# Performance work log

Measured on AMD Instinct MI355X. Metric: run time of the kernel, lower is better.

Reference implementation:

```python
import jax, jax.numpy as jnp
import numpy as np

B, T, D, H, L, S = 128, 100, 256, 512, 40000, 10  # batch, steps, input_size, hidden_size, loc_count, num_slots


def setup_inputs() -> dict:
    key = jax.random.key(0)
    ks = jax.random.split(key, 24)
    stdv = 1.0 / np.sqrt(H)
    u = lambda k, shape: jax.random.uniform(k, shape, jnp.float32, -stdv, stdv)
    inp = {
        "batch_l": jax.random.randint(ks[0], (B, T), 0, L),
        "t_ld": jax.random.uniform(ks[1], (B, T), jnp.float32),
        "t_hd": jax.random.uniform(ks[2], (B, T), jnp.float32),
        "t_l": jax.random.randint(ks[3], (B, T), 0, S),
        "t_h": jax.random.randint(ks[4], (B, T), 0, S),
        "d_ld": jax.random.uniform(ks[5], (B, T), jnp.float32),
        "d_hd": jax.random.uniform(ks[6], (B, T), jnp.float32),
        "d_l": jax.random.randint(ks[7], (B, T), 0, S),
        "d_h": jax.random.randint(ks[8], (B, T), 0, S),
        # learned parameters
        "embed_l": jax.random.normal(ks[9], (L, D), jnp.float32) * 0.02,
        "embed_s": jax.random.normal(ks[10], (S, D), jnp.float32) * 0.02,
        "embed_q": jax.random.normal(ks[11], (S, D), jnp.float32) * 0.02,
        "w_ih": u(ks[12], (4 * H, D)),
        "w_hh": u(ks[13], (4 * H, H)),
        "w_s": u(ks[14], (3 * H, D)),
        "w_q": u(ks[15], (3 * H, D)),
        "b_ih": u(ks[16], (4 * H,)),
        "b_hh": u(ks[17], (4 * H,)),
        "w_out": u(ks[18], (L, H)),
        "b_out": u(ks[19], (L,)),
    }
    return inp


def reference(batch_l, t_ld, t_hd, t_l, t_h, d_ld, d_hd, d_l, d_h,
              embed_l, embed_s, embed_q, w_ih, w_hh, w_s, w_q,
              b_ih, b_hh, w_out, b_out):
    # embedding lookups + slot interpolation: lower_embed*hd + higher_embed*ld
    xl = embed_l[batch_l]                                           # (B,T,D)
    xs = embed_s[d_l] * d_hd[..., None] + embed_s[d_h] * d_ld[..., None]
    xq = embed_q[t_l] * t_hd[..., None] + embed_q[t_h] * t_ld[..., None]

    def step(hc, x):
        h, c = hc
        xl_t, xs_t, xq_t = x                                        # each (B,D)
        gates = xl_t @ w_ih.T + h @ w_hh.T + b_ih + b_hh            # (B,4H)
        i, f, g, o = jnp.split(gates, 4, axis=1)
        sq = xs_t @ w_s.T + xq_t @ w_q.T                            # (B,3H), order (i,f,o)
        si, sf, so = jnp.split(sq, 3, axis=1)
        i = jax.nn.sigmoid(i + si)
        f = jax.nn.sigmoid(f + sf)
        o = jax.nn.sigmoid(o + so)
        g = jnp.tanh(g)
        c2 = f * c + i * g
        h2 = o * jnp.tanh(g)  # faithful to source: tanh(cell_gate), not tanh(next_cell)
        return (h2, c2), None

    h0 = jnp.zeros((B, H), xl.dtype)
    (hT, cT), _ = jax.lax.scan(
        step, (h0, h0),
        (xl.transpose(1, 0, 2), xs.transpose(1, 0, 2), xq.transpose(1, 0, 2)))
    # classifier on last hidden state
    return hT @ w_out.T + b_out                                     # (B,L)
```

## Files before the change

### kernel.cpp

```cpp
#include <hip/hip_runtime.h>

#define B_ 128
#define T_ 100
#define D_ 256
#define H_ 512
#define L_ 40000
#define S_ 10

__device__ __forceinline__ float sigm_(float x){ return 1.f/(1.f + __expf(-x)); }
__device__ __forceinline__ float tanh_(float x){ return 1.f - 2.f/(__expf(2.f*x) + 1.f); }

typedef __attribute__((ext_vector_type(8))) short bf16x8;
typedef __attribute__((ext_vector_type(4))) float f32x4;

__device__ __forceinline__ unsigned short bfhi_(float x){
  unsigned u = __float_as_uint(x);
  return (unsigned short)((u + 0x7FFFu + ((u >> 16) & 1u)) >> 16);
}
__device__ __forceinline__ float bf2f_(unsigned short h){
  return __uint_as_float(((unsigned)h) << 16);
}
__device__ __forceinline__ float decp_(unsigned u){
  return bf2f_((unsigned short)(u & 0xFFFFu)) + bf2f_((unsigned short)(u >> 16));
}

__global__ void k_init(unsigned long long* __restrict__ h_enc, unsigned* __restrict__ flags,
                       const float* __restrict__ embed_s, const float* __restrict__ embed_q,
                       const float* __restrict__ w_s, const float* __restrict__ w_q,
                       float* __restrict__ es_proj, float* __restrict__ eq_proj){
  int bid = blockIdx.x, tid = threadIdx.x;
  if (bid < 256){ h_enc[bid*256 + tid] = 0ull; return; }
  if (bid == 256){ if (tid < 256) flags[tid] = 0u; return; }
  int b2 = bid - 257;
  int table = b2/20, rem = b2%20, s = rem/2, half = rem%2;
  int jo = half*256 + tid;
  const float* emb = (table ? embed_q : embed_s) + s*D_;
  const float* w   = (table ? w_q : w_s) + (size_t)(2*H_ + jo)*D_;
  float acc = 0.f;
  #pragma unroll 4
  for (int k=0;k<D_;++k) acc = fmaf(emb[k], w[k], acc);
  (table ? eq_proj : es_proj)[s*H_ + jo] = acc;
}

__global__ __launch_bounds__(256) void k_conv_w(
  const float* __restrict__ w_ih,
  unsigned short* __restrict__ Whi, unsigned short* __restrict__ Wlo)
{
  int g = blockIdx.x*256 + threadIdx.x;
  size_t row = (size_t)(g >> 6), k4 = (size_t)(g & 63)*4;
  const float* src = w_ih + (2*H_ + row)*D_ + k4;
  size_t off = row*D_ + k4;
  float4 v = *(const float4*)src;
  ushort4 hi, lo;
  hi.x = bfhi_(v.x); lo.x = bfhi_(v.x - bf2f_(hi.x));
  hi.y = bfhi_(v.y); lo.y = bfhi_(v.y - bf2f_(hi.y));
  hi.z = bfhi_(v.z); lo.z = bfhi_(v.z - bf2f_(hi.z));
  hi.w = bfhi_(v.w); lo.w = bfhi_(v.w - bf2f_(hi.w));
  *(ushort4*)(Whi + off) = hi;
  *(ushort4*)(Wlo + off) = lo;
}

__global__ __launch_bounds__(256) void k_phase1(
  const int* __restrict__ batch_l, const float* __restrict__ embed_l,
  const unsigned short* __restrict__ Whi, const unsigned short* __restrict__ Wlo,
  const float* __restrict__ b_ih, const float* __restrict__ b_hh,
  const float* __restrict__ t_ld, const float* __restrict__ t_hd,
  const int* __restrict__ t_l, const int* __restrict__ t_h,
  const float* __restrict__ d_ld, const float* __restrict__ d_hd,
  const int* __restrict__ d_l, const int* __restrict__ d_h,
  const float* __restrict__ es_proj, const float* __restrict__ eq_proj,
  float* __restrict__ P)
{
  __shared__ int ridx[64];
  int mt = blockIdx.x, jt = blockIdx.y;
  int t = mt >> 1, b0 = (mt & 1)*64;
  int tid = threadIdx.x;
  if (tid < 64) ridx[tid] = batch_l[(b0+tid)*T_ + t];
  __syncthreads();

  int lane = tid & 63, wv = tid >> 6;
  int ar = lane & 15, kb = lane >> 4;
  int mw = wv*16;
  f32x4 acc0 = {0.f,0.f,0.f,0.f}, acc1 = {0.f,0.f,0.f,0.f};
  f32x4 acc2 = {0.f,0.f,0.f,0.f}, acc3 = {0.f,0.f,0.f,0.f};
  const float* arow_f = embed_l + (size_t)ridx[mw + ar]*D_ + kb*8;
  const size_t brow0 = (size_t)(jt*64 + ar)*D_ + kb*8;
  #pragma unroll
  for (int kc=0; kc<8; ++kc){
    float4 f0 = *(const float4*)(arow_f + kc*32);
    float4 f1 = *(const float4*)(arow_f + kc*32 + 4);
    float vv[8] = {f0.x,f0.y,f0.z,f0.w,f1.x,f1.y,f1.z,f1.w};
    bf16x8 a_hi, a_lo;
    #pragma unroll
    for (int i=0;i<8;++i){
      unsigned short h = bfhi_(vv[i]);
      a_hi[i] = (short)h;
      a_lo[i] = (short)bfhi_(vv[i] - bf2f_(h));
    }
    #pragma unroll
    for (int nf=0; nf<4; ++nf){
      bf16x8 b_hi = *(const bf16x8*)(Whi + brow0 + (size_t)nf*16*D_ + kc*32);
      bf16x8 b_lo = *(const bf16x8*)(Wlo + brow0 + (size_t)nf*16*D_ + kc*32);
      f32x4 a = (nf==0)?acc0:(nf==1)?acc1:(nf==2)?acc2:acc3;
      a = __builtin_amdgcn_mfma_f32_16x16x32_bf16(a_hi, b_hi, a, 0, 0, 0);
      a = __builtin_amdgcn_mfma_f32_16x16x32_bf16(a_hi, b_lo, a, 0, 0, 0);
      a = __builtin_amdgcn_mfma_f32_16x16x32_bf16(a_lo, b_hi, a, 0, 0, 0);
      if (nf==0) acc0=a; else if (nf==1) acc1=a; else if (nf==2) acc2=a; else acc3=a;
    }
  }

  float bias[4];
  #pragma unroll
  for (int nf=0; nf<4; ++nf){
    int j = jt*64 + nf*16 + ar;
    bias[nf] = b_ih[2*H_ + j] + b_hh[2*H_ + j];
  }
  #pragma unroll
  for (int r=0; r<4; ++r){
    int b = b0 + mw + kb*4 + r;
    float dldv=0.f, dhdv=0.f, tldv=0.f, thdv=0.f;
    int dlv=0, dhv=0, tlv=0, thv=0;
    if (jt >= 8){
      int bt = b*T_ + t;
      dldv=d_ld[bt]; dhdv=d_hd[bt]; tldv=t_ld[bt]; thdv=t_hd[bt];
      dlv=d_l[bt]; dhv=d_h[bt]; tlv=t_l[bt]; thv=t_h[bt];
    }
    #pragma unroll
    for (int nf=0; nf<4; ++nf){
      int j = jt*64 + nf*16 + ar;
      float v = ((nf==0)?acc0[r]:(nf==1)?acc1[r]:(nf==2)?acc2[r]:acc3[r]) + bias[nf];
      if (jt >= 8){
        int jo = j - 512;
        v += dhdv*es_proj[dlv*H_+jo] + dldv*es_proj[dhv*H_+jo]
           + thdv*eq_proj[tlv*H_+jo] + tldv*eq_proj[thv*H_+jo];
      }
      P[((size_t)t*B_ + b)*1024 + j] = v;
    }
  }
}

__global__ __launch_bounds__(256,1) void k_rec(
  const float* __restrict__ w_hh, const float* __restrict__ P,
  unsigned long long* __restrict__ h_enc, unsigned* __restrict__ flags)
{
  extern __shared__ char smc[];
  unsigned short* Whi = (unsigned short*)smc;
  unsigned short* Wlo = Whi + 64*528;
  unsigned* hb = (unsigned*)(Wlo + 64*528);
  int bid = blockIdx.x;
  int bg = bid & 15, js = bid >> 4;
  int tid = threadIdx.x;
  int lane = tid & 63, wv = tid >> 6;
  const int gb0 = bg*8;
  unsigned* bgflags = flags + bg*16;

  {
    int r = tid >> 2;
    int c0 = (tid & 3)*128;
    int rr = r & 15;
    int jrow = js*32 + (r>>4)*8 + (rr & 7);
    const float* src = w_hh + (size_t)(((rr<8)?2:3)*H_ + jrow)*H_ + c0;
    unsigned short* dhi = Whi + r*528 + c0;
    unsigned short* dlo = Wlo + r*528 + c0;
    #pragma unroll 4
    for (int i=0;i<32;++i){
      float4 v = *(const float4*)(src + i*4);
      ushort4 hi, lo;
      hi.x=bfhi_(v.x); lo.x=bfhi_(v.x-bf2f_(hi.x));
      hi.y=bfhi_(v.y); lo.y=bfhi_(v.y-bf2f_(hi.y));
      hi.z=bfhi_(v.z); lo.z=bfhi_(v.z-bf2f_(hi.z));
      hi.w=bfhi_(v.w); lo.w=bfhi_(v.w-bf2f_(hi.w));
      *(ushort4*)(dhi + i*4) = hi;
      *(ushort4*)(dlo + i*4) = lo;
    }
  }

  const bool live = (lane < 32) && ((lane & 15) < 8);
  int bb = lane & 15;
  int j0l = js*32 + wv*8 + (lane>>4)*4;
  float pgv[4] = {0,0,0,0}, pov[4] = {0,0,0,0};
  if (live){
    size_t prow = (size_t)(gb0 + bb)*1024;
    float4 g4 = *(const float4*)&P[prow + j0l];
    float4 o4 = *(const float4*)&P[prow + 512 + j0l];
    pgv[0]=g4.x; pgv[1]=g4.y; pgv[2]=g4.z; pgv[3]=g4.w;
    pov[0]=o4.x; pov[1]=o4.y; pov[2]=o4.z; pov[3]=o4.w;
  }
  const int arow_off = (wv*16 + (lane & 15))*528 + (lane>>4)*8;
  const int hcol = lane & 7;
  const int hk0 = (lane>>4)*8;

  for (int t=0; t<T_; ++t){
    int par = t & 1;
    if (t > 0 && tid < 16){
      unsigned* f = bgflags + tid;
      int guard = 0;
      while (__hip_atomic_load(f, __ATOMIC_RELAXED, __HIP_MEMORY_SCOPE_AGENT) < (unsigned)t){
        __builtin_amdgcn_s_sleep(4);
        if (++guard > (1<<22)) break;
      }
    }
    __syncthreads();

    const unsigned long long* hsrc =
      h_enc + (size_t)par*(B_*H_/2) + (size_t)gb0*256 + tid;
    unsigned long long v[8];
    #pragma unroll
    for (int b=0;b<8;++b)
      v[b] = __hip_atomic_load(&hsrc[(size_t)b*256], __ATOMIC_RELAXED, __HIP_MEMORY_SCOPE_AGENT);
    {
      unsigned* r0 = hb + (2*tid)*10;
      unsigned* r1 = hb + (2*tid+1)*10;
      *(uint4*)(r0+0) = make_uint4((unsigned)v[0],(unsigned)v[1],(unsigned)v[2],(unsigned)v[3]);
      *(uint4*)(r0+4) = make_uint4((unsigned)v[4],(unsigned)v[5],(unsigned)v[6],(unsigned)v[7]);
      *(uint2*)(r1+0) = make_uint2((unsigned)(v[0]>>32),(unsigned)(v[1]>>32));
      *(uint2*)(r1+2) = make_uint2((unsigned)(v[2]>>32),(unsigned)(v[3]>>32));
      *(uint2*)(r1+4) = make_uint2((unsigned)(v[4]>>32),(unsigned)(v[5]>>32));
      *(uint2*)(r1+6) = make_uint2((unsigned)(v[6]>>32),(unsigned)(v[7]>>32));
    }
    __syncthreads();

    f32x4 ac0 = {0,0,0,0}, ac1 = {0,0,0,0}, ac2 = {0,0,0,0};
    #pragma unroll
    for (int kc=0; kc<16; ++kc){
      bf16x8 bh, bl;
      #pragma unroll
      for (int e=0;e<8;++e){
        unsigned u = hb[(kc*32 + hk0 + e)*10 + hcol];
        bh[e] = (short)(u & 0xFFFFu);
        bl[e] = (short)(u >> 16);
      }
      bf16x8 ah = *(const bf16x8*)(Whi + arow_off + kc*32);
      bf16x8 al = *(const bf16x8*)(Wlo + arow_off + kc*32);
      ac0 = __builtin_amdgcn_mfma_f32_16x16x32_bf16(ah, bh, ac0, 0, 0, 0);
      ac1 = __builtin_amdgcn_mfma_f32_16x16x32_bf16(ah, bl, ac1, 0, 0, 0);
      ac2 = __builtin_amdgcn_mfma_f32_16x16x32_bf16(al, bh, ac2, 0, 0, 0);
    }
    float accv[4], oov[4];
    #pragma unroll
    for (int r=0;r<4;++r) accv[r] = ac0[r] + ac1[r] + ac2[r];
    #pragma unroll
    for (int r=0;r<4;++r) oov[r] = __shfl_xor(accv[r], 32, 64);

    if (live){
      float h[4];
      #pragma unroll
      for (int r=0;r<4;++r){
        float gg = accv[r] + pgv[r];
        float oo = oov[r]  + pov[r];
        h[r] = sigm_(oo)*tanh_(tanh_(gg));
      }
      unsigned short p0h=bfhi_(h[0]), p0l=bfhi_(h[0]-bf2f_(p0h));
      unsigned short p1h=bfhi_(h[1]), p1l=bfhi_(h[1]-bf2f_(p1h));
      unsigned short p2h=bfhi_(h[2]), p2l=bfhi_(h[2]-bf2f_(p2h));
      unsigned short p3h=bfhi_(h[3]), p3l=bfhi_(h[3]-bf2f_(p3h));
      unsigned long long u0 = (unsigned long long)p0h | ((unsigned long long)p0l<<16)
                            | ((unsigned long long)p1h<<32) | ((unsigned long long)p1l<<48);
      unsigned long long u1 = (unsigned long long)p2h | ((unsigned long long)p2l<<16)
                            | ((unsigned long long)p3h<<32) | ((unsigned long long)p3l<<48);
      unsigned long long* dst =
        h_enc + (size_t)(1-par)*(B_*H_/2) + (size_t)(gb0 + bb)*256 + (j0l>>1);
      __hip_atomic_store(dst,   u0, __ATOMIC_RELAXED, __HIP_MEMORY_SCOPE_AGENT);
      __hip_atomic_store(dst+1, u1, __ATOMIC_RELAXED, __HIP_MEMORY_SCOPE_AGENT);
      if (t+1 < T_){
        size_t prow = ((size_t)(t+1)*B_ + gb0 + bb)*1024;
        float4 g4 = *(const float4*)&P[prow + j0l];
        float4 o4 = *(const float4*)&P[prow + 512 + j0l];
        pgv[0]=g4.x; pgv[1]=g4.y; pgv[2]=g4.z; pgv[3]=g4.w;
        pov[0]=o4.x; pov[1]=o4.y; pov[2]=o4.z; pov[3]=o4.w;
      }
    }
    __syncthreads();
    if (t+1 < T_ && tid == 0)
      __hip_atomic_store(bgflags + js, (unsigned)(t+1),
                         __ATOMIC_RELAXED, __HIP_MEMORY_SCOPE_AGENT);
  }
}

__global__ __launch_bounds__(256) void k_cls(
  const unsigned long long* __restrict__ h_enc, const float* __restrict__ w_out,
  const float* __restrict__ b_out, float* __restrict__ out)
{
  __shared__ float wt[32*68];
  __shared__ float htl[32*132];
  int l0 = blockIdx.x * 64;
  int tid = threadIdx.x;
  int lq = tid >> 4, bq = tid & 15;
  float acc[4][8] = {};
  for (int kc=0; kc<16; ++kc){
    int k0 = kc*32;
    __syncthreads();
    #pragma unroll
    for (int it=0; it<2; ++it){
      int f = it*256 + tid;
      int l = f >> 3, k4 = (f & 7)*4;
      float4 v = *(const float4*)&w_out[(size_t)(l0+l)*H_ + k0 + k4];
      wt[(k4+0)*68 + l] = v.x; wt[(k4+1)*68 + l] = v.y;
      wt[(k4+2)*68 + l] = v.z; wt[(k4+3)*68 + l] = v.w;
    }
    #pragma unroll
    for (int it=0; it<4; ++it){
      int f = it*256 + tid;
      int b = f >> 3, k4 = (f & 7)*4;
      uint4 v = *(const uint4*)&h_enc[(size_t)b*256 + ((k0 + k4) >> 1)];
      htl[(k4+0)*132 + b] = decp_(v.x);
      htl[(k4+1)*132 + b] = decp_(v.y);
      htl[(k4+2)*132 + b] = decp_(v.z);
      htl[(k4+3)*132 + b] = decp_(v.w);
    }
    __syncthreads();
    #pragma unroll 4
    for (int k=0;k<32;++k){
      float4 w4 = *(const float4*)&wt[k*68 + lq*4];
      float4 h0 = *(const float4*)&htl[k*132 + bq*8];
      float4 h1 = *(const float4*)&htl[k*132 + bq*8 + 4];
      float wv[4] = {w4.x,w4.y,w4.z,w4.w};
      float hv[8] = {h0.x,h0.y,h0.z,h0.w,h1.x,h1.y,h1.z,h1.w};
      #pragma unroll
      for (int m=0;m<4;++m)
        #pragma unroll
        for (int i=0;i<8;++i) acc[m][i] = fmaf(wv[m], hv[i], acc[m][i]);
    }
  }
  int l = l0 + lq*4;
  float4 bo = *(const float4*)&b_out[l];
  #pragma unroll
  for (int i=0;i<8;++i){
    int b = bq*8 + i;
    float4 o4;
    o4.x = acc[0][i] + bo.x; o4.y = acc[1][i] + bo.y;
    o4.z = acc[2][i] + bo.z; o4.w = acc[3][i] + bo.w;
    *(float4*)&out[(size_t)b*L_ + l] = o4;
  }
}

extern "C" void kernel_launch(void* const* d_in, const int* in_sizes, int n_in,
                              void* d_out, int out_size, void* d_ws, size_t ws_size,
                              hipStream_t stream) {
  const int*   batch_l = (const int*)  d_in[0];
  const float* t_ld    = (const float*)d_in[1];
  const float* t_hd    = (const float*)d_in[2];
  const int*   t_l     = (const int*)  d_in[3];
  const int*   t_h     = (const int*)  d_in[4];
  const float* d_ld    = (const float*)d_in[5];
  const float* d_hd    = (const float*)d_in[6];
  const int*   d_l     = (const int*)  d_in[7];
  const int*   d_h     = (const int*)  d_in[8];
  const float* embed_l = (const float*)d_in[9];
  const float* embed_s = (const float*)d_in[10];
  const float* embed_q = (const float*)d_in[11];
  const float* w_ih    = (const float*)d_in[12];
  const float* w_hh    = (const float*)d_in[13];
  const float* w_s     = (const float*)d_in[14];
  const float* w_q     = (const float*)d_in[15];
  const float* b_ih    = (const float*)d_in[16];
  const float* b_hh    = (const float*)d_in[17];
  const float* w_out   = (const float*)d_in[18];
  const float* b_out   = (const float*)d_in[19];
  float* out = (float*)d_out;

  float* ws = (float*)d_ws;
  const size_t P_off   = 0;
  const size_t h_off   = 13107200;
  const size_t es_off  = h_off + 131072;
  const size_t eq_off  = es_off + 5120;
  const size_t flg_off = eq_off + 5120;
  const size_t whi_off = flg_off + 256;
  const size_t wlo_off = whi_off + 131072;
  const size_t need_base = (flg_off + 256)*4 + 64;
  const size_t need_full = (wlo_off + 131072)*4 + 64;
  if (ws_size < need_base) return;

  float* P        = ws + P_off;
  unsigned long long* h_enc = (unsigned long long*)(ws + h_off);
  float* es_proj  = ws + es_off;
  float* eq_proj  = ws + eq_off;
  unsigned* flags = (unsigned*)(ws + flg_off);
  unsigned short* Whi = (unsigned short*)(ws + whi_off);
  unsigned short* Wlo = (unsigned short*)(ws + wlo_off);

  hipFuncSetAttribute(reinterpret_cast<const void*>(k_rec),
                      hipFuncAttributeMaxDynamicSharedMemorySize, 155648);

  k_init<<<297, 256, 0, stream>>>(h_enc, flags, embed_s, embed_q, w_s, w_q,
                                  es_proj, eq_proj);
  if (ws_size >= need_full){
    k_conv_w<<<256, 256, 0, stream>>>(w_ih, Whi, Wlo);
    k_phase1<<<dim3(200,16), 256, 0, stream>>>(batch_l, embed_l, Whi, Wlo,
        b_ih, b_hh, t_ld, t_hd, t_l, t_h, d_ld, d_hd, d_l, d_h, es_proj, eq_proj, P);
  } else {
    return;
  }
  k_rec<<<256, 256, 155648, stream>>>(w_hh, P, h_enc, flags);
  k_cls<<<625, 256, 0, stream>>>(h_enc, w_out, b_out, out);
}
```

Measured before the change: 558.9 us.

## Widen phase1 column tile per block and repack h buffer layout in recurrence

The input-projection kernel now has each block compute 256 output columns with 16 accumulators instead of 64 columns with 4. This reuses the converted embedding A fragments across four times as many MFMAs and cuts the grid from 3200 to 800 blocks, at the cost of higher register pressure under launch_bounds(256,2). The recurrent kernel's shared h staging buffer is repacked to an 18-word row stride per thread, which changes LDS bank access patterns and slightly shrinks dynamic shared memory. The host fallback branch is folded into a single workspace-size check.

```diff
diff --git a/kernel.cpp b/kernel.cpp
--- a/kernel.cpp
+++ b/kernel.cpp
@@ -60,7 +60,7 @@
   *(ushort4*)(Wlo + off) = lo;
 }
 
-__global__ __launch_bounds__(256) void k_phase1(
+__global__ __launch_bounds__(256,2) void k_phase1(
   const int* __restrict__ batch_l, const float* __restrict__ embed_l,
   const unsigned short* __restrict__ Whi, const unsigned short* __restrict__ Wlo,
   const float* __restrict__ b_ih, const float* __restrict__ b_hh,
@@ -72,7 +72,7 @@
   float* __restrict__ P)
 {
   __shared__ int ridx[64];
-  int mt = blockIdx.x, jt = blockIdx.y;
+  int mt = blockIdx.x, jg = blockIdx.y;
   int t = mt >> 1, b0 = (mt & 1)*64;
   int tid = threadIdx.x;
   if (tid < 64) ridx[tid] = batch_l[(b0+tid)*T_ + t];
@@ -81,10 +81,11 @@
   int lane = tid & 63, wv = tid >> 6;
   int ar = lane & 15, kb = lane >> 4;
   int mw = wv*16;
-  f32x4 acc0 = {0.f,0.f,0.f,0.f}, acc1 = {0.f,0.f,0.f,0.f};
-  f32x4 acc2 = {0.f,0.f,0.f,0.f}, acc3 = {0.f,0.f,0.f,0.f};
+  f32x4 acc[16];
+  #pragma unroll
+  for (int nf=0;nf<16;++nf) acc[nf] = (f32x4){0.f,0.f,0.f,0.f};
   const float* arow_f = embed_l + (size_t)ridx[mw + ar]*D_ + kb*8;
-  const size_t brow0 = (size_t)(jt*64 + ar)*D_ + kb*8;
+  const size_t brow0 = (size_t)(jg*256 + ar)*D_ + kb*8;
   #pragma unroll
   for (int kc=0; kc<8; ++kc){
     float4 f0 = *(const float4*)(arow_f + kc*32);
@@ -98,21 +99,19 @@
       a_lo[i] = (short)bfhi_(vv[i] - bf2f_(h));
     }
     #pragma unroll
-    for (int nf=0; nf<4; ++nf){
+    for (int nf=0; nf<16; ++nf){
       bf16x8 b_hi = *(const bf16x8*)(Whi + brow0 + (size_t)nf*16*D_ + kc*32);
       bf16x8 b_lo = *(const bf16x8*)(Wlo + brow0 + (size_t)nf*16*D_ + kc*32);
-      f32x4 a = (nf==0)?acc0:(nf==1)?acc1:(nf==2)?acc2:acc3;
-      a = __builtin_amdgcn_mfma_f32_16x16x32_bf16(a_hi, b_hi, a, 0, 0, 0);
-      a = __builtin_amdgcn_mfma_f32_16x16x32_bf16(a_hi, b_lo, a, 0, 0, 0);
-      a = __builtin_amdgcn_mfma_f32_16x16x32_bf16(a_lo, b_hi, a, 0, 0, 0);
-      if (nf==0) acc0=a; else if (nf==1) acc1=a; else if (nf==2) acc2=a; else acc3=a;
-    }
-  }
-
-  float bias[4];
-  #pragma unroll
-  for (int nf=0; nf<4; ++nf){
-    int j = jt*64 + nf*16 + ar;
+      acc[nf] = __builtin_amdgcn_mfma_f32_16x16x32_bf16(a_hi, b_hi, acc[nf], 0, 0, 0);
+      acc[nf] = __builtin_amdgcn_mfma_f32_16x16x32_bf16(a_hi, b_lo, acc[nf], 0, 0, 0);
+      acc[nf] = __builtin_amdgcn_mfma_f32_16x16x32_bf16(a_lo, b_hi, acc[nf], 0, 0, 0);
+    }
+  }
+
+  float bias[16];
+  #pragma unroll
+  for (int nf=0; nf<16; ++nf){
+    int j = jg*256 + nf*16 + ar;
     bias[nf] = b_ih[2*H_ + j] + b_hh[2*H_ + j];
   }
   #pragma unroll
@@ -120,16 +119,16 @@
     int b = b0 + mw + kb*4 + r;
     float dldv=0.f, dhdv=0.f, tldv=0.f, thdv=0.f;
     int dlv=0, dhv=0, tlv=0, thv=0;
-    if (jt >= 8){
+    if (jg >= 2){
       int bt = b*T_ + t;
       dldv=d_ld[bt]; dhdv=d_hd[bt]; tldv=t_ld[bt]; thdv=t_hd[bt];
       dlv=d_l[bt]; dhv=d_h[bt]; tlv=t_l[bt]; thv=t_h[bt];
     }
     #pragma unroll
-    for (int nf=0; nf<4; ++nf){
-      int j = jt*64 + nf*16 + ar;
-      float v = ((nf==0)?acc0[r]:(nf==1)?acc1[r]:(nf==2)?acc2[r]:acc3[r]) + bias[nf];
-      if (jt >= 8){
+    for (int nf=0; nf<16; ++nf){
+      int j = jg*256 + nf*16 + ar;
+      float v = acc[nf][r] + bias[nf];
+      if (jg >= 2){
         int jo = j - 512;
         v += dhdv*es_proj[dlv*H_+jo] + dldv*es_proj[dhv*H_+jo]
            + thdv*eq_proj[tlv*H_+jo] + tldv*eq_proj[thv*H_+jo];
@@ -188,7 +187,7 @@
   }
   const int arow_off = (wv*16 + (lane & 15))*528 + (lane>>4)*8;
   const int hcol = lane & 7;
-  const int hk0 = (lane>>4)*8;
+  const int hp0 = (lane>>4)*4;
 
   for (int t=0; t<T_; ++t){
     int par = t & 1;
@@ -209,14 +208,15 @@
     for (int b=0;b<8;++b)
       v[b] = __hip_atomic_load(&hsrc[(size_t)b*256], __ATOMIC_RELAXED, __HIP_MEMORY_SCOPE_AGENT);
     {
-      unsigned* r0 = hb + (2*tid)*10;
-      unsigned* r1 = hb + (2*tid+1)*10;
-      *(uint4*)(r0+0) = make_uint4((unsigned)v[0],(unsigned)v[1],(unsigned)v[2],(unsigned)v[3]);
-      *(uint4*)(r0+4) = make_uint4((unsigned)v[4],(unsigned)v[5],(unsigned)v[6],(unsigned)v[7]);
-      *(uint2*)(r1+0) = make_uint2((unsigned)(v[0]>>32),(unsigned)(v[1]>>32));
-      *(uint2*)(r1+2) = make_uint2((unsigned)(v[2]>>32),(unsigned)(v[3]>>32));
-      *(uint2*)(r1+4) = make_uint2((unsigned)(v[4]>>32),(unsigned)(v[5]>>32));
-      *(uint2*)(r1+6) = make_uint2((unsigned)(v[6]>>32),(unsigned)(v[7]>>32));
+      unsigned* r0 = hb + tid*18;
+      *(uint2*)(r0+ 0) = make_uint2((unsigned)v[0],(unsigned)v[1]);
+      *(uint2*)(r0+ 2) = make_uint2((unsigned)v[2],(unsigned)v[3]);
+      *(uint2*)(r0+ 4) = make_uint2((unsigned)v[4],(unsigned)v[5]);
+      *(uint2*)(r0+ 6) = make_uint2((unsigned)v[6],(unsigned)v[7]);
+      *(uint2*)(r0+ 8) = make_uint2((unsigned)(v[0]>>32),(unsigned)(v[1]>>32));
+      *(uint2*)(r0+10) = make_uint2((unsigned)(v[2]>>32),(unsigned)(v[3]>>32));
+      *(uint2*)(r0+12) = make_uint2((unsigned)(v[4]>>32),(unsigned)(v[5]>>32));
+      *(uint2*)(r0+14) = make_uint2((unsigned)(v[6]>>32),(unsigned)(v[7]>>32));
     }
     __syncthreads();
 
@@ -226,7 +226,7 @@
       bf16x8 bh, bl;
       #pragma unroll
       for (int e=0;e<8;++e){
-        unsigned u = hb[(kc*32 + hk0 + e)*10 + hcol];
+        unsigned u = hb[(kc*16 + hp0 + (e>>1))*18 + (e&1)*8 + hcol];
         bh[e] = (short)(u & 0xFFFFu);
         bl[e] = (short)(u >> 16);
       }
@@ -367,9 +367,8 @@
   const size_t flg_off = eq_off + 5120;
   const size_t whi_off = flg_off + 256;
   const size_t wlo_off = whi_off + 131072;
-  const size_t need_base = (flg_off + 256)*4 + 64;
   const size_t need_full = (wlo_off + 131072)*4 + 64;
-  if (ws_size < need_base) return;
+  if (ws_size < need_full) return;
 
   float* P        = ws + P_off;
   unsigned long long* h_enc = (unsigned long long*)(ws + h_off);
@@ -380,17 +379,13 @@
   unsigned short* Wlo = (unsigned short*)(ws + wlo_off);
 
   hipFuncSetAttribute(reinterpret_cast<const void*>(k_rec),
-                      hipFuncAttributeMaxDynamicSharedMemorySize, 155648);
+                      hipFuncAttributeMaxDynamicSharedMemorySize, 153600);
 
   k_init<<<297, 256, 0, stream>>>(h_enc, flags, embed_s, embed_q, w_s, w_q,
                                   es_proj, eq_proj);
-  if (ws_size >= need_full){
-    k_conv_w<<<256, 256, 0, stream>>>(w_ih, Whi, Wlo);
-    k_phase1<<<dim3(200,16), 256, 0, stream>>>(batch_l, embed_l, Whi, Wlo,
-        b_ih, b_hh, t_ld, t_hd, t_l, t_h, d_ld, d_hd, d_l, d_h, es_proj, eq_proj, P);
-  } else {
-    return;
-  }
-  k_rec<<<256, 256, 155648, stream>>>(w_hh, P, h_enc, flags);
+  k_conv_w<<<256, 256, 0, stream>>>(w_ih, Whi, Wlo);
+  k_phase1<<<dim3(200,4), 256, 0, stream>>>(batch_l, embed_l, Whi, Wlo,
+      b_ih, b_hh, t_ld, t_hd, t_l, t_h, d_ld, d_hd, d_l, d_h, es_proj, eq_proj, P);
+  k_rec<<<256, 256, 153600, stream>>>(w_hh, P, h_enc, flags);
   k_cls<<<625, 256, 0, stream>>>(h_enc, w_out, b_out, out);
 }
```

Result: no change. 564.3 us (+1.0%).
